# Performance work log

Hardware: AMD Instinct MI355X
Metric: run time of the kernel (lower is better)

The kernel has to match this reference:

```python
import jax, jax.numpy as jnp
import numpy as np

N, K, M, DIM = 131072, 16, 128, 64


def setup_inputs() -> dict:
    key = jax.random.key(0)
    kx, ks, ka, kb = jax.random.split(key, 4)
    return {
        "x": jax.random.normal(kx, (N, DIM), dtype=jnp.float32),
        "s": jax.random.normal(ks, (K,), dtype=jnp.float32),
        "a": jax.random.normal(ka, (K, M, DIM), dtype=jnp.float32),
        "b": jax.random.normal(kb, (K, M), dtype=jnp.float32),
    }


def reference(x, s, a, b):
    # scores[k, n, m] = x[n, :] @ a[k, m, :] + b[k, m]  (batched GEMM over k)
    scores = jnp.einsum("nd,kmd->knm", x, a) + b[:, None, :]
    # per-expert logsumexp over the m affine pieces -> [k, n]
    lse = jax.nn.logsumexp(scores, axis=-1)
    # signed sum over experts -> [n]
    return jnp.einsum("k,kn->n", s, lse)
```

## Files before the change

kernel.cpp:

```cpp
#include <hip/hip_runtime.h>
#include <hip/hip_bf16.h>

#define NROWS 131072
#define KEXP 16
#define MPC 128
#define DIMD 64

typedef float f32x4 __attribute__((ext_vector_type(4)));
typedef short s16x8 __attribute__((ext_vector_type(8)));

#define L2E 1.4426950408889634f
#define LN2 0.6931471805599453f
#define BIAS_OFF 262144

static __device__ inline unsigned int b2u(__hip_bfloat162 h) {
    union { __hip_bfloat162 h; unsigned int u; } c;
    c.h = h;
    return c.u;
}

static __device__ inline int4 cvt8s(float4 f0, float4 f1, float sc) {
    __hip_bfloat162 p0 = __float22bfloat162_rn(make_float2(f0.x * sc, f0.y * sc));
    __hip_bfloat162 p1 = __float22bfloat162_rn(make_float2(f0.z * sc, f0.w * sc));
    __hip_bfloat162 p2 = __float22bfloat162_rn(make_float2(f1.x * sc, f1.y * sc));
    __hip_bfloat162 p3 = __float22bfloat162_rn(make_float2(f1.z * sc, f1.w * sc));
    int4 pk;
    pk.x = (int)b2u(p0); pk.y = (int)b2u(p1); pk.z = (int)b2u(p2); pk.w = (int)b2u(p3);
    return pk;
}

static __device__ inline void async_copy16(const void* g, void* l) {
    __builtin_amdgcn_global_load_lds(
        (const __attribute__((address_space(1))) unsigned int*)g,
        (__attribute__((address_space(3))) unsigned int*)l, 16, 0, 0);
}

__global__ void prep_kernel(const float* __restrict__ a, const float* __restrict__ b,
                            short* __restrict__ abff, float* __restrict__ out) {
    const int u = blockIdx.x * 256 + threadIdx.x;
    if (u < 16384) {
        const int k  = u >> 10;
        const int c2 = (u >> 6) & 15;
        const int ul = u & 63;
        const int mt = c2 >> 1;
        const int kc = c2 & 1;
        const float* p = a + (size_t)(k * MPC + mt * 16 + (ul & 15)) * DIMD
                           + kc * 32 + (ul >> 4) * 8;
        int4 pk = cvt8s(*(const float4*)(p), *(const float4*)(p + 4), L2E);
        *(int4*)(abff + (size_t)u * 8) = pk;
    } else if (u < 16384 + 2048) {
        const int v = u - 16384;
        ((float*)((char*)abff + BIAS_OFF))[v] = b[v] * L2E;
    }
    for (int i = u; i < NROWS; i += 80 * 256) out[i] = 0.f;
}

__global__ __launch_bounds__(256, 8)
void fused_kernel(const float* __restrict__ x, const float* __restrict__ s,
                  const short* __restrict__ abff, float* __restrict__ out) {
    __shared__ int4 abuf[2][512];

    const int tid = threadIdx.x;
    const int w   = tid >> 6;
    const int l   = tid & 63;
    const int lq  = l >> 4;

    const int family = blockIdx.x & 1;
    const int r0     = (blockIdx.x >> 1) * 64 + w * 16;

    const int kf0 = family * 8;
    const char* ab = (const char*)abff;
    const float* bs = (const float*)(ab + BIAS_OFF);

    {
        const char* src = ab + (size_t)kf0 * 16384 + l * 16;
        async_copy16(src + w * 1024,       (char*)&abuf[0][0] + w * 1024);
        async_copy16(src + (w + 4) * 1024, (char*)&abuf[0][0] + (w + 4) * 1024);
    }

    union { int4 i; s16x8 v; } Bf[2];
#pragma unroll
    for (int kc = 0; kc < 2; ++kc) {
        const float* gp = x + (size_t)(r0 + (l & 15)) * DIMD + kc * 32 + lq * 8;
        float4 f0 = *(const float4*)(gp);
        float4 f1 = *(const float4*)(gp + 4);
        Bf[kc].i = cvt8s(f0, f1, 1.0f);
    }

    __syncthreads();

    float racc = 0.f;

    for (int k = 0; k < 8; ++k) {
        const int kf = kf0 + k;
        const float sk2 = s[kf] * LN2;
        float e0 = 0.f, e1 = 0.f, e2 = 0.f, e3 = 0.f;

        {
            const char* src = ab + (size_t)kf * 16384 + 8192 + l * 16;
            async_copy16(src + w * 1024,       (char*)&abuf[1][0] + w * 1024);
            async_copy16(src + (w + 4) * 1024, (char*)&abuf[1][0] + (w + 4) * 1024);
        }
#pragma unroll
        for (int mtl = 0; mtl < 4; ++mtl) {
            const char* base = (const char*)&abuf[0][0] + mtl * 2048 + l * 16;
            f32x4 acc = *(const f32x4*)(bs + kf * MPC + mtl * 16 + lq * 4);
            s16x8 Af0 = *(const s16x8*)(base);
            acc = __builtin_amdgcn_mfma_f32_16x16x32_bf16(Af0, Bf[0].v, acc, 0, 0, 0);
            s16x8 Af1 = *(const s16x8*)(base + 1024);
            acc = __builtin_amdgcn_mfma_f32_16x16x32_bf16(Af1, Bf[1].v, acc, 0, 0, 0);
            e0 += __builtin_amdgcn_exp2f(acc[0]);
            e1 += __builtin_amdgcn_exp2f(acc[1]);
            e2 += __builtin_amdgcn_exp2f(acc[2]);
            e3 += __builtin_amdgcn_exp2f(acc[3]);
        }
        __syncthreads();

        if (k < 7) {
            const char* src = ab + (size_t)(kf + 1) * 16384 + l * 16;
            async_copy16(src + w * 1024,       (char*)&abuf[0][0] + w * 1024);
            async_copy16(src + (w + 4) * 1024, (char*)&abuf[0][0] + (w + 4) * 1024);
        }
#pragma unroll
        for (int mtl = 0; mtl < 4; ++mtl) {
            const char* base = (const char*)&abuf[1][0] + mtl * 2048 + l * 16;
            f32x4 acc = *(const f32x4*)(bs + kf * MPC + 64 + mtl * 16 + lq * 4);
            s16x8 Af0 = *(const s16x8*)(base);
            acc = __builtin_amdgcn_mfma_f32_16x16x32_bf16(Af0, Bf[0].v, acc, 0, 0, 0);
            s16x8 Af1 = *(const s16x8*)(base + 1024);
            acc = __builtin_amdgcn_mfma_f32_16x16x32_bf16(Af1, Bf[1].v, acc, 0, 0, 0);
            e0 += __builtin_amdgcn_exp2f(acc[0]);
            e1 += __builtin_amdgcn_exp2f(acc[1]);
            e2 += __builtin_amdgcn_exp2f(acc[2]);
            e3 += __builtin_amdgcn_exp2f(acc[3]);
        }

        float tot = (e0 + e1) + (e2 + e3);
        tot += __shfl_xor(tot, 16);
        tot += __shfl_xor(tot, 32);
        racc = fmaf(sk2, __log2f(tot), racc);

        __syncthreads();
    }

    if (l < 16)
        atomicAdd(&out[r0 + l], racc);
}

extern "C" void kernel_launch(void* const* d_in, const int* in_sizes, int n_in,
                              void* d_out, int out_size, void* d_ws, size_t ws_size,
                              hipStream_t stream) {
    const float* x = (const float*)d_in[0];
    const float* s = (const float*)d_in[1];
    const float* a = (const float*)d_in[2];
    const float* b = (const float*)d_in[3];
    float* out = (float*)d_out;

    short* abff = (short*)d_ws;

    prep_kernel<<<80, 256, 0, stream>>>(a, b, abff, out);
    fused_kernel<<<NROWS / 32, 256, 0, stream>>>(x, s, abff, out);
}
```

Baseline: 135.3 us.

## Process two row tiles per wave and stage bias through LDS

Each wave now handles 32 rows (two 16-row MFMA tiles), so every expert tile of A staged in LDS is reused across twice as many rows, and the grid is halved. The bias is re-laid out in prep and async-copied into LDS next to the A chunks instead of being read from global memory per MFMA group. This cuts LDS traffic, A reloads and per-block sync overhead per row, at the cost of more registers per thread and fewer blocks, which may reduce occupancy and latency hiding.

```diff
diff --git a/kernel.cpp b/kernel.cpp
--- a/kernel.cpp
+++ b/kernel.cpp
@@ -50,7 +50,10 @@
         *(int4*)(abff + (size_t)u * 8) = pk;
     } else if (u < 16384 + 2048) {
         const int v = u - 16384;
-        ((float*)((char*)abff + BIAS_OFF))[v] = b[v] * L2E;
+        const int k = v >> 7;
+        const int m = v & 127;
+        float* bf = (float*)((char*)abff + BIAS_OFF);
+        bf[(size_t)(k * 2 + (m >> 6)) * 256 + (m & 63)] = b[k * MPC + m] * L2E;
     }
     for (int i = u; i < NROWS; i += 80 * 256) out[i] = 0.f;
 }
@@ -58,7 +61,7 @@
 __global__ __launch_bounds__(256, 8)
 void fused_kernel(const float* __restrict__ x, const float* __restrict__ s,
                   const short* __restrict__ abff, float* __restrict__ out) {
-    __shared__ int4 abuf[2][512];
+    __shared__ int4 abuf[2][576];
 
     const int tid = threadIdx.x;
     const int w   = tid >> 6;
@@ -66,85 +69,127 @@
     const int lq  = l >> 4;
 
     const int family = blockIdx.x & 1;
-    const int r0     = (blockIdx.x >> 1) * 64 + w * 16;
+    const int r0     = (blockIdx.x >> 1) * 128 + w * 32;
 
     const int kf0 = family * 8;
     const char* ab = (const char*)abff;
-    const float* bs = (const float*)(ab + BIAS_OFF);
 
     {
-        const char* src = ab + (size_t)kf0 * 16384 + l * 16;
-        async_copy16(src + w * 1024,       (char*)&abuf[0][0] + w * 1024);
-        async_copy16(src + (w + 4) * 1024, (char*)&abuf[0][0] + (w + 4) * 1024);
-    }
-
-    union { int4 i; s16x8 v; } Bf[2];
-#pragma unroll
-    for (int kc = 0; kc < 2; ++kc) {
-        const float* gp = x + (size_t)(r0 + (l & 15)) * DIMD + kc * 32 + lq * 8;
-        float4 f0 = *(const float4*)(gp);
-        float4 f1 = *(const float4*)(gp + 4);
-        Bf[kc].i = cvt8s(f0, f1, 1.0f);
-    }
+        const char* srcA = ab + (size_t)kf0 * 16384 + l * 16;
+        const char* srcB = ab + BIAS_OFF + (size_t)kf0 * 2048 + l * 16;
+#pragma unroll
+        for (int i = 0; i < 3; ++i) {
+            const int ch = w + 4 * i;
+            if (ch < 8)
+                async_copy16(srcA + ch * 1024, (char*)&abuf[0][0] + ch * 1024);
+            else if (ch == 8)
+                async_copy16(srcB, (char*)&abuf[0][0] + 8192);
+        }
+    }
+
+    union { int4 i; s16x8 v; } Bf[2][2];
+#pragma unroll
+    for (int nt = 0; nt < 2; ++nt)
+#pragma unroll
+        for (int kc = 0; kc < 2; ++kc) {
+            const float* gp = x + (size_t)(r0 + nt * 16 + (l & 15)) * DIMD
+                                + kc * 32 + lq * 8;
+            float4 f0 = *(const float4*)(gp);
+            float4 f1 = *(const float4*)(gp + 4);
+            Bf[nt][kc].i = cvt8s(f0, f1, 1.0f);
+        }
 
     __syncthreads();
 
-    float racc = 0.f;
+    float racc0 = 0.f, racc1 = 0.f;
 
     for (int k = 0; k < 8; ++k) {
         const int kf = kf0 + k;
         const float sk2 = s[kf] * LN2;
-        float e0 = 0.f, e1 = 0.f, e2 = 0.f, e3 = 0.f;
+        float e0 = 0.f, e1 = 0.f;
 
         {
-            const char* src = ab + (size_t)kf * 16384 + 8192 + l * 16;
-            async_copy16(src + w * 1024,       (char*)&abuf[1][0] + w * 1024);
-            async_copy16(src + (w + 4) * 1024, (char*)&abuf[1][0] + (w + 4) * 1024);
+            const char* srcA = ab + (size_t)kf * 16384 + 8192 + l * 16;
+            const char* srcB = ab + BIAS_OFF + (size_t)kf * 2048 + 1024 + l * 16;
+#pragma unroll
+            for (int i = 0; i < 3; ++i) {
+                const int ch = w + 4 * i;
+                if (ch < 8)
+                    async_copy16(srcA + ch * 1024, (char*)&abuf[1][0] + ch * 1024);
+                else if (ch == 8)
+                    async_copy16(srcB, (char*)&abuf[1][0] + 8192);
+            }
         }
 #pragma unroll
         for (int mtl = 0; mtl < 4; ++mtl) {
-            const char* base = (const char*)&abuf[0][0] + mtl * 2048 + l * 16;
-            f32x4 acc = *(const f32x4*)(bs + kf * MPC + mtl * 16 + lq * 4);
-            s16x8 Af0 = *(const s16x8*)(base);
-            acc = __builtin_amdgcn_mfma_f32_16x16x32_bf16(Af0, Bf[0].v, acc, 0, 0, 0);
-            s16x8 Af1 = *(const s16x8*)(base + 1024);
-            acc = __builtin_amdgcn_mfma_f32_16x16x32_bf16(Af1, Bf[1].v, acc, 0, 0, 0);
-            e0 += __builtin_amdgcn_exp2f(acc[0]);
-            e1 += __builtin_amdgcn_exp2f(acc[1]);
-            e2 += __builtin_amdgcn_exp2f(acc[2]);
-            e3 += __builtin_amdgcn_exp2f(acc[3]);
+            const char* Ab = (const char*)&abuf[0][0];
+            f32x4 bv = *(const f32x4*)(Ab + 8192 + mtl * 64 + lq * 16);
+            f32x4 acc0 = bv, acc1 = bv;
+            s16x8 Af0 = *(const s16x8*)(Ab + (mtl * 2 + 0) * 1024 + l * 16);
+            acc0 = __builtin_amdgcn_mfma_f32_16x16x32_bf16(Af0, Bf[0][0].v, acc0, 0, 0, 0);
+            acc1 = __builtin_amdgcn_mfma_f32_16x16x32_bf16(Af0, Bf[1][0].v, acc1, 0, 0, 0);
+            s16x8 Af1 = *(const s16x8*)(Ab + (mtl * 2 + 1) * 1024 + l * 16);
+            acc0 = __builtin_amdgcn_mfma_f32_16x16x32_bf16(Af1, Bf[0][1].v, acc0, 0, 0, 0);
+            acc1 = __builtin_amdgcn_mfma_f32_16x16x32_bf16(Af1, Bf[1][1].v, acc1, 0, 0, 0);
+            e0 += __builtin_amdgcn_exp2f(acc0[0]);
+            e0 += __builtin_amdgcn_exp2f(acc0[1]);
+            e0 += __builtin_amdgcn_exp2f(acc0[2]);
+            e0 += __builtin_amdgcn_exp2f(acc0[3]);
+            e1 += __builtin_amdgcn_exp2f(acc1[0]);
+            e1 += __builtin_amdgcn_exp2f(acc1[1]);
+            e1 += __builtin_amdgcn_exp2f(acc1[2]);
+            e1 += __builtin_amdgcn_exp2f(acc1[3]);
         }
         __syncthreads();
 
         if (k < 7) {
-            const char* src = ab + (size_t)(kf + 1) * 16384 + l * 16;
-            async_copy16(src + w * 1024,       (char*)&abuf[0][0] + w * 1024);
-            async_copy16(src + (w + 4) * 1024, (char*)&abuf[0][0] + (w + 4) * 1024);
+            const char* srcA = ab + (size_t)(kf + 1) * 16384 + l * 16;
+            const char* srcB = ab + BIAS_OFF + (size_t)(kf + 1) * 2048 + l * 16;
+#pragma unroll
+            for (int i = 0; i < 3; ++i) {
+                const int ch = w + 4 * i;
+                if (ch < 8)
+                    async_copy16(srcA + ch * 1024, (char*)&abuf[0][0] + ch * 1024);
+                else if (ch == 8)
+                    async_copy16(srcB, (char*)&abuf[0][0] + 8192);
+            }
         }
 #pragma unroll
         for (int mtl = 0; mtl < 4; ++mtl) {
-            const char* base = (const char*)&abuf[1][0] + mtl * 2048 + l * 16;
-            f32x4 acc = *(const f32x4*)(bs + kf * MPC + 64 + mtl * 16 + lq * 4);
-            s16x8 Af0 = *(const s16x8*)(base);
-            acc = __builtin_amdgcn_mfma_f32_16x16x32_bf16(Af0, Bf[0].v, acc, 0, 0, 0);
-            s16x8 Af1 = *(const s16x8*)(base + 1024);
-            acc = __builtin_amdgcn_mfma_f32_16x16x32_bf16(Af1, Bf[1].v, acc, 0, 0, 0);
-            e0 += __builtin_amdgcn_exp2f(acc[0]);
-            e1 += __builtin_amdgcn_exp2f(acc[1]);
-            e2 += __builtin_amdgcn_exp2f(acc[2]);
-            e3 += __builtin_amdgcn_exp2f(acc[3]);
-        }
-
-        float tot = (e0 + e1) + (e2 + e3);
-        tot += __shfl_xor(tot, 16);
-        tot += __shfl_xor(tot, 32);
-        racc = fmaf(sk2, __log2f(tot), racc);
+            const char* Ab = (const char*)&abuf[1][0];
+            f32x4 bv = *(const f32x4*)(Ab + 8192 + mtl * 64 + lq * 16);
+            f32x4 acc0 = bv, acc1 = bv;
+            s16x8 Af0 = *(const s16x8*)(Ab + (mtl * 2 + 0) * 1024 + l * 16);
+            acc0 = __builtin_amdgcn_mfma_f32_16x16x32_bf16(Af0, Bf[0][0].v, acc0, 0, 0, 0);
+            acc1 = __builtin_amdgcn_mfma_f32_16x16x32_bf16(Af0, Bf[1][0].v, acc1, 0, 0, 0);
+            s16x8 Af1 = *(const s16x8*)(Ab + (mtl * 2 + 1) * 1024 + l * 16);
+            acc0 = __builtin_amdgcn_mfma_f32_16x16x32_bf16(Af1, Bf[0][1].v, acc0, 0, 0, 0);
+            acc1 = __builtin_amdgcn_mfma_f32_16x16x32_bf16(Af1, Bf[1][1].v, acc1, 0, 0, 0);
+            e0 += __builtin_amdgcn_exp2f(acc0[0]);
+            e0 += __builtin_amdgcn_exp2f(acc0[1]);
+            e0 += __builtin_amdgcn_exp2f(acc0[2]);
+            e0 += __builtin_amdgcn_exp2f(acc0[3]);
+            e1 += __builtin_amdgcn_exp2f(acc1[0]);
+            e1 += __builtin_amdgcn_exp2f(acc1[1]);
+            e1 += __builtin_amdgcn_exp2f(acc1[2]);
+            e1 += __builtin_amdgcn_exp2f(acc1[3]);
+        }
+
+        float tot0 = e0, tot1 = e1;
+        tot0 += __shfl_xor(tot0, 16);
+        tot0 += __shfl_xor(tot0, 32);
+        tot1 += __shfl_xor(tot1, 16);
+        tot1 += __shfl_xor(tot1, 32);
+        racc0 = fmaf(sk2, __log2f(tot0), racc0);
+        racc1 = fmaf(sk2, __log2f(tot1), racc1);
 
         __syncthreads();
     }
 
-    if (l < 16)
-        atomicAdd(&out[r0 + l], racc);
+    if (l < 16) {
+        atomicAdd(&out[r0 + l], racc0);
+        atomicAdd(&out[r0 + 16 + l], racc1);
+    }
 }
 
 extern "C" void kernel_launch(void* const* d_in, const int* in_sizes, int n_in,
@@ -159,5 +204,5 @@
     short* abff = (short*)d_ws;
 
     prep_kernel<<<80, 256, 0, stream>>>(a, b, abff, out);
-    fused_kernel<<<NROWS / 32, 256, 0, stream>>>(x, s, abff, out);
-}
+    fused_kernel<<<NROWS / 64, 256, 0, stream>>>(x, s, abff, out);
+}
```

Result: no change. 133.2 us (-1.5%).
